# Performance work log

Hardware: AMD Instinct MI355X
Metric: run time of the kernel (lower is better)

## Reference

```python
import jax, jax.numpy as jnp
import numpy as np

N_NODES = 50000
N_EDGES = 800000
IN_FEATS = 256
N_HIDDEN = 256
N_CLASSES = 47


def _glorot(key, shape):
    fan_in, fan_out = shape
    lim = (6.0 / (fan_in + fan_out)) ** 0.5
    return jax.random.uniform(key, shape, jnp.float32, -lim, lim)


def setup_inputs() -> dict:
    key = jax.random.key(0)
    ks = jax.random.split(key, 12)
    x = jax.random.normal(ks[0], (N_NODES, IN_FEATS), jnp.float32)
    src = jax.random.randint(ks[1], (N_EDGES,), 0, N_NODES, jnp.int64)
    dst = jax.random.randint(ks[2], (N_EDGES,), 0, N_NODES, jnp.int64)
    dims = [(IN_FEATS, N_HIDDEN), (N_HIDDEN, N_HIDDEN), (N_HIDDEN, N_CLASSES)]
    inp = {"x": x, "src": src, "dst": dst}
    for i, (di, do) in enumerate(dims):
        inp[f"Wself{i}"] = _glorot(ks[3 + 3 * i], (di, do))
        inp[f"Wneigh{i}"] = _glorot(ks[4 + 3 * i], (di, do))
        inp[f"b{i}"] = jnp.zeros((do,), jnp.float32)
    return inp


def _sage_layer(h, src, dst, Ws, Wn, b):
    # DGL mean SAGEConv: fc_self(h) + fc_neigh(mean over in-neighbors) + bias
    msum = jax.ops.segment_sum(h[src], dst, num_segments=N_NODES)      # [N, d]
    deg = jax.ops.segment_sum(jnp.ones((src.shape[0],), h.dtype), dst,
                              num_segments=N_NODES)                     # [N]
    hmean = msum / jnp.maximum(deg, 1.0)[:, None]
    return h @ Ws + hmean @ Wn + b


def reference(x, src, dst, Wself0, Wneigh0, b0, Wself1, Wneigh1, b1,
              Wself2, Wneigh2, b2):
    h = _sage_layer(x, src, dst, Wself0, Wneigh0, b0)
    h = jax.nn.selu(h)
    h = _sage_layer(h, src, dst, Wself1, Wneigh1, b1)
    h = jax.nn.selu(h)
    h = _sage_layer(h, src, dst, Wself2, Wneigh2, b2)
    return jax.nn.softmax(h, axis=1)
```

## Files before the change

kernel.cpp:

```cpp
#include <hip/hip_runtime.h>
#include <math.h>

#define FEATS 256
#define KTOT  512
#define MS    264
#define SA    40

typedef __attribute__((ext_vector_type(8))) __bf16 bf16x8;
typedef __attribute__((ext_vector_type(4))) float f32x4;

__device__ __forceinline__ float bf2f(unsigned short u) {
    union { unsigned int i; float f; } v; v.i = ((unsigned int)u) << 16; return v.f;
}
__device__ __forceinline__ unsigned short f2bf(float f) {
    unsigned int u = __float_as_uint(f);
    unsigned int r = (u + 0x7FFFu + ((u >> 16) & 1u)) >> 16;
    return (unsigned short)r;
}

__global__ void k_detect(const int* __restrict__ srcRaw, const unsigned short* __restrict__ xr,
                         int nE, int* __restrict__ flag) {
    __shared__ int any, cnt;
    if (threadIdx.x == 0) { any = 0; cnt = 0; }
    __syncthreads();
    int lim = nE < 1024 ? nE : 1024;
    for (int i = threadIdx.x; i < lim; i += 256)
        if (srcRaw[2 * i + 1] != 0) atomicAdd(&any, 1);
    int loc = 0;
    for (int i = threadIdx.x; i < 1024; i += 256) {
        unsigned e = (xr[2 * i] >> 7) & 255u;
        if (e >= 90u && e <= 140u) loc++;
    }
    atomicAdd(&cnt, loc);
    __syncthreads();
    if (threadIdx.x == 0) {
        flag[0] = (any == 0) ? 1 : 0;
        flag[1] = (cnt > 512) ? 1 : 0;
    }
}

__global__ void k_count(const int* __restrict__ dstRaw, int* __restrict__ deg, int nE,
                        int nNodes, const int* __restrict__ flag) {
    int e = blockIdx.x * 256 + threadIdx.x;
    if (e >= nE) return;
    int f = flag[0];
    int d = dstRaw[f ? (2 * e) : e];
    if ((unsigned)d >= (unsigned)nNodes) d = 0;
    atomicAdd(&deg[d], 1);
}

__global__ __launch_bounds__(256) void k_bsum(const int* __restrict__ deg, int* __restrict__ bsum,
                                              int n) {
    __shared__ int buf[256];
    const int t = threadIdx.x;
    int i = blockIdx.x * 256 + t;
    buf[t] = (i < n) ? deg[i] : 0;
    __syncthreads();
    for (int s = 128; s > 0; s >>= 1) {
        if (t < s) buf[t] += buf[t + s];
        __syncthreads();
    }
    if (t == 0) bsum[blockIdx.x] = buf[0];
}

__global__ __launch_bounds__(256) void k_scanb(int* __restrict__ bsum, int nB) {
    __shared__ int buf[256];
    __shared__ int carry;
    const int t = threadIdx.x;
    if (t == 0) carry = 0;
    __syncthreads();
    for (int base = 0; base < nB; base += 256) {
        int i = base + t;
        int v = (i < nB) ? bsum[i] : 0;
        buf[t] = v;
        __syncthreads();
        for (int s = 1; s < 256; s <<= 1) {
            int tv = (t >= s) ? buf[t - s] : 0;
            __syncthreads();
            buf[t] += tv;
            __syncthreads();
        }
        int exc = buf[t] - v;
        int c = carry;
        if (i < nB) bsum[i] = c + exc;
        int tot = buf[255];
        __syncthreads();
        if (t == 0) carry = c + tot;
        __syncthreads();
    }
}

__global__ __launch_bounds__(256) void k_offs(const int* __restrict__ deg,
                                              const int* __restrict__ bsum,
                                              int* __restrict__ off, int* __restrict__ cursor,
                                              int n) {
    __shared__ int buf[256];
    const int t = threadIdx.x, b = blockIdx.x;
    int i = b * 256 + t;
    int v = (i < n) ? deg[i] : 0;
    buf[t] = v;
    __syncthreads();
    for (int s = 1; s < 256; s <<= 1) {
        int tv = (t >= s) ? buf[t - s] : 0;
        __syncthreads();
        buf[t] += tv;
        __syncthreads();
    }
    int exc = bsum[b] + buf[t] - v;
    if (i < n) { off[i] = exc; cursor[i] = exc; }
    if (i == n - 1) off[n] = exc + v;
}

__global__ void k_fill(const int* __restrict__ srcRaw, const int* __restrict__ dstRaw,
                       int* __restrict__ cursor, int* __restrict__ csr, int nE,
                       int nNodes, const int* __restrict__ flag) {
    int e = blockIdx.x * 256 + threadIdx.x;
    if (e >= nE) return;
    int f = flag[0];
    int d = dstRaw[f ? (2 * e) : e];
    int s = srcRaw[f ? (2 * e) : e];
    if ((unsigned)d >= (unsigned)nNodes) d = 0;
    if ((unsigned)s >= (unsigned)nNodes) s = 0;
    int pos = atomicAdd(&cursor[d], 1);
    csr[pos] = s;
}

template <bool F32>
__global__ void k_buildWt(const void* __restrict__ Ws, const void* __restrict__ Wn,
                          unsigned short* __restrict__ Wt, int N, int Npad,
                          const int* __restrict__ flag) {
    if (flag[1] != (F32 ? 0 : 1)) return;
    int idx = blockIdx.x * 256 + threadIdx.x;
    if (idx >= Npad * KTOT) return;
    int n = idx >> 9, k = idx & 511;
    unsigned short v = 0;
    if (n < N) {
        if (F32) {
            float fv = (k < 256) ? ((const float*)Ws)[k * N + n]
                                 : ((const float*)Wn)[(k - 256) * N + n];
            v = f2bf(fv);
        } else {
            v = (k < 256) ? ((const unsigned short*)Ws)[k * N + n]
                          : ((const unsigned short*)Wn)[(k - 256) * N + n];
        }
    }
    Wt[idx] = v;
}

template <bool F32>
__global__ void k_buildWt1(const void* __restrict__ W, unsigned short* __restrict__ Wt,
                           int N, const int* __restrict__ flag) {
    if (flag[1] != (F32 ? 0 : 1)) return;
    int idx = blockIdx.x * 256 + threadIdx.x;
    if (idx >= 64 * 256) return;
    int n = idx >> 8, k = idx & 255;
    unsigned short v = 0;
    if (n < N) {
        v = F32 ? f2bf(((const float*)W)[k * N + n])
                : ((const unsigned short*)W)[k * N + n];
    }
    Wt[idx] = v;
}

template <bool F32>
__device__ __forceinline__ void stage8(const void* h, size_t elemOff, unsigned short* dst) {
    if (!F32) {
        *reinterpret_cast<float4*>(dst) =
            *reinterpret_cast<const float4*>((const unsigned short*)h + elemOff);
    } else {
        const float* p = (const float*)h + elemOff;
        float4 a = *reinterpret_cast<const float4*>(p);
        float4 b = *reinterpret_cast<const float4*>(p + 4);
        dst[0] = f2bf(a.x); dst[1] = f2bf(a.y); dst[2] = f2bf(a.z); dst[3] = f2bf(a.w);
        dst[4] = f2bf(b.x); dst[5] = f2bf(b.y); dst[6] = f2bf(b.z); dst[7] = f2bf(b.w);
    }
}

template <bool HF32>
__global__ __launch_bounds__(256) void k_aggr(
        const void* __restrict__ h, const int* __restrict__ off,
        const int* __restrict__ csr, unsigned short* __restrict__ hmean,
        int M, const int* __restrict__ flag, int want) {
    if (want >= 0 && flag[1] != want) return;
    const int lane = threadIdx.x & 63;
    const int wid = (blockIdx.x * 256 + threadIdx.x) >> 6;
    const int nw = (gridDim.x * 256) >> 6;
    for (int r = wid; r < M; r += nw) {
        const int e0 = off[r], e1 = off[r + 1];
        float a0 = 0.f, a1 = 0.f, a2 = 0.f, a3 = 0.f;
        for (int base = e0; base < e1; base += 64) {
            int cnt = e1 - base; if (cnt > 64) cnt = 64;
            int sidx = (lane < cnt) ? csr[base + lane] : 0;
            #pragma unroll 8
            for (int d = 0; d < cnt; d++) {
                int s = __shfl(sidx, d);
                if (HF32) {
                    float4 hv = reinterpret_cast<const float4*>(
                        (const float*)h + (size_t)s * FEATS)[lane];
                    a0 += hv.x; a1 += hv.y; a2 += hv.z; a3 += hv.w;
                } else {
                    ushort4 hv = reinterpret_cast<const ushort4*>(
                        (const unsigned short*)h + (size_t)s * FEATS)[lane];
                    a0 += bf2f(hv.x); a1 += bf2f(hv.y); a2 += bf2f(hv.z); a3 += bf2f(hv.w);
                }
            }
        }
        float rc = 1.0f / fmaxf((float)(e1 - e0), 1.0f);
        ushort4 o;
        o.x = f2bf(a0 * rc); o.y = f2bf(a1 * rc); o.z = f2bf(a2 * rc); o.w = f2bf(a3 * rc);
        *reinterpret_cast<ushort4*>(&hmean[(size_t)r * FEATS + lane * 4]) = o;
    }
}

__global__ __launch_bounds__(256) void k_aggrP(
        const unsigned short* __restrict__ P, const int* __restrict__ off,
        const int* __restrict__ csr, unsigned short* __restrict__ A, int M) {
    const int lane = threadIdx.x & 63;
    const int wid = (blockIdx.x * 256 + threadIdx.x) >> 6;
    const int nw = (gridDim.x * 256) >> 6;
    const int g = lane >> 5, li = lane & 31;
    for (int r = wid; r < M; r += nw) {
        const int e0 = off[r], e1 = off[r + 1];
        float a0 = 0.f, a1 = 0.f;
        #pragma unroll 4
        for (int base = e0; base < e1; base += 2) {
            int e = base + g;
            if (e < e1) {
                int s = csr[e];
                ushort2 hv = *reinterpret_cast<const ushort2*>(
                    P + (size_t)s * 64 + li * 2);
                a0 += bf2f(hv.x); a1 += bf2f(hv.y);
            }
        }
        a0 += __shfl_xor(a0, 32); a1 += __shfl_xor(a1, 32);
        if (g == 0) {
            float rc = 1.0f / fmaxf((float)(e1 - e0), 1.0f);
            unsigned int packed = (unsigned int)f2bf(a0 * rc) |
                                  ((unsigned int)f2bf(a1 * rc) << 16);
            *reinterpret_cast<unsigned int*>(&A[(size_t)r * 64 + li * 2]) = packed;
        }
    }
}

template <int NT, int ACT, bool HF32, bool BF32, bool OF32>
__global__ __launch_bounds__(256) void k_gemm(
        const void* __restrict__ h, const unsigned short* __restrict__ hmean,
        const unsigned short* __restrict__ Wt, const void* __restrict__ bias,
        void* __restrict__ out, int M, int C, const int* __restrict__ flag, int want) {
    if (flag[1] != want) return;
    __shared__ __align__(16) unsigned short As[64 * SA];
    __shared__ __align__(16) unsigned short Bs[NT * 16 * SA];

    const int m0 = blockIdx.x * 64;
    const int tid = threadIdx.x;
    const int lane = tid & 63, w = tid >> 6;
    const int nh = lane & 15, q = lane >> 4;

    f32x4 acc[NT];
    #pragma unroll
    for (int ci = 0; ci < NT; ci++) acc[ci] = (f32x4){0.f, 0.f, 0.f, 0.f};

    for (int kb = 0; kb < KTOT; kb += 32) {
        {
            int row = tid >> 2, seg = tid & 3;
            int gr = m0 + row; if (gr > M - 1) gr = M - 1;
            if (kb < 256)
                stage8<HF32>(h, (size_t)gr * FEATS + kb + seg * 8, &As[row * SA + seg * 8]);
            else
                stage8<false>(hmean, (size_t)gr * FEATS + (kb - 256) + seg * 8,
                              &As[row * SA + seg * 8]);
        }
        for (int u = tid; u < NT * 64; u += 256) {
            int nn = u >> 2, seg = u & 3;
            *reinterpret_cast<float4*>(&Bs[nn * SA + seg * 8]) =
                *reinterpret_cast<const float4*>(Wt + (size_t)nn * KTOT + kb + seg * 8);
        }
        __syncthreads();
        bf16x8 afr = *reinterpret_cast<const bf16x8*>(&As[(w * 16 + nh) * SA + q * 8]);
        #pragma unroll
        for (int ci = 0; ci < NT; ci++) {
            bf16x8 bfr = *reinterpret_cast<const bf16x8*>(&Bs[(ci * 16 + nh) * SA + q * 8]);
            acc[ci] = __builtin_amdgcn_mfma_f32_16x16x32_bf16(afr, bfr, acc[ci], 0, 0, 0);
        }
        __syncthreads();
    }

    const int rbase = m0 + w * 16 + q * 4;
    const float sc = 1.0507009873554805f, al = 1.6732632423543772f;
    #pragma unroll
    for (int ci = 0; ci < NT; ci++) {
        int col = ci * 16 + nh;
        float b = BF32 ? ((const float*)bias)[col] : bf2f(((const unsigned short*)bias)[col]);
        #pragma unroll
        for (int rg = 0; rg < 4; rg++) {
            int r = rbase + rg;
            if (r < M) {
                float v = acc[ci][rg] + b;
                v = (v > 0.f) ? sc * v : sc * al * expm1f(v);
                if (OF32) ((float*)out)[(size_t)r * (NT * 16) + col] = v;
                else ((unsigned short*)out)[(size_t)r * (NT * 16) + col] = f2bf(v);
            }
        }
    }
}

template <int NT, int ACT, bool ADDP, bool BF32, bool OF32>
__global__ __launch_bounds__(256) void k_gemm256(
        const unsigned short* __restrict__ h, const unsigned short* __restrict__ Wt,
        const void* __restrict__ bias, const unsigned short* __restrict__ Padd,
        void* __restrict__ out, int M, int C, const int* __restrict__ flag, int want) {
    if (want >= 0 && flag[1] != want) return;
    __shared__ __align__(16) unsigned short As[64 * SA];
    __shared__ __align__(16) unsigned short Bs[NT * 16 * SA];

    const int m0 = blockIdx.x * 64;
    const int tid = threadIdx.x;
    const int lane = tid & 63, w = tid >> 6;
    const int nh = lane & 15, q = lane >> 4;

    f32x4 acc[NT];
    #pragma unroll
    for (int ci = 0; ci < NT; ci++) acc[ci] = (f32x4){0.f, 0.f, 0.f, 0.f};

    for (int kb = 0; kb < 256; kb += 32) {
        {
            int row = tid >> 2, seg = tid & 3;
            int gr = m0 + row; if (gr > M - 1) gr = M - 1;
            stage8<false>(h, (size_t)gr * FEATS + kb + seg * 8, &As[row * SA + seg * 8]);
        }
        for (int u = tid; u < NT * 64; u += 256) {
            int nn = u >> 2, seg = u & 3;
            *reinterpret_cast<float4*>(&Bs[nn * SA + seg * 8]) =
                *reinterpret_cast<const float4*>(Wt + (size_t)nn * 256 + kb + seg * 8);
        }
        __syncthreads();
        bf16x8 afr = *reinterpret_cast<const bf16x8*>(&As[(w * 16 + nh) * SA + q * 8]);
        #pragma unroll
        for (int ci = 0; ci < NT; ci++) {
            bf16x8 bfr = *reinterpret_cast<const bf16x8*>(&Bs[(ci * 16 + nh) * SA + q * 8]);
            acc[ci] = __builtin_amdgcn_mfma_f32_16x16x32_bf16(afr, bfr, acc[ci], 0, 0, 0);
        }
        __syncthreads();
    }

    const int rbase = m0 + w * 16 + q * 4;
    if (ACT == 2) {
        #pragma unroll
        for (int ci = 0; ci < NT; ci++) {
            int col = ci * 16 + nh;
            #pragma unroll
            for (int rg = 0; rg < 4; rg++) {
                int r = rbase + rg;
                if (r < M)
                    ((unsigned short*)out)[(size_t)r * (NT * 16) + col] = f2bf(acc[ci][rg]);
            }
        }
    } else {
        #pragma unroll
        for (int rg = 0; rg < 4; rg++) {
            int r = rbase + rg;
            int rr = (r < M) ? r : (M - 1);
            float vals[NT];
            float mx = -1e30f;
            #pragma unroll
            for (int ci = 0; ci < NT; ci++) {
                int col = ci * 16 + nh;
                float v = -1e30f;
                if (col < C) {
                    float b = BF32 ? ((const float*)bias)[col] : bf2f(((const unsigned short*)bias)[col]);
                    float a = ADDP ? bf2f(Padd[(size_t)rr * 64 + col]) : 0.f;
                    v = acc[ci][rg] + a + b;
                }
                vals[ci] = v;
                mx = fmaxf(mx, v);
            }
            #pragma unroll
            for (int mk = 1; mk <= 8; mk <<= 1) mx = fmaxf(mx, __shfl_xor(mx, mk));
            float s = 0.f;
            #pragma unroll
            for (int ci = 0; ci < NT; ci++) {
                float e = (vals[ci] <= -1e29f) ? 0.f : __expf(vals[ci] - mx);
                vals[ci] = e; s += e;
            }
            #pragma unroll
            for (int mk = 1; mk <= 8; mk <<= 1) s += __shfl_xor(s, mk);
            float inv = 1.f / s;
            if (r < M) {
                #pragma unroll
                for (int ci = 0; ci < NT; ci++) {
                    int col = ci * 16 + nh;
                    if (col < C) {
                        if (OF32) ((float*)out)[(size_t)r * C + col] = vals[ci] * inv;
                        else ((unsigned short*)out)[(size_t)r * C + col] = f2bf(vals[ci] * inv);
                    }
                }
            }
        }
    }
}

template <int NT, int ACT, bool HF32, bool BF32, bool OF32>
__global__ __launch_bounds__(256) void k_sage(
        const void* __restrict__ h, const int* __restrict__ off,
        const int* __restrict__ csr, const unsigned short* __restrict__ Wt,
        const void* __restrict__ bias, void* __restrict__ out,
        int M, int C, const int* __restrict__ flag, int want) {
    if (flag[1] != want) return;
    __shared__ __align__(16) unsigned short meanS[64 * MS];
    __shared__ __align__(16) unsigned short As[64 * SA];
    __shared__ __align__(16) unsigned short Bs[NT * 16 * SA];

    const int m0 = blockIdx.x * 64;
    const int tid = threadIdx.x;
    const int lane = tid & 63, w = tid >> 6;
    const int nh = lane & 15, q = lane >> 4;

    for (int i = 0; i < 16; i++) {
        int lr = w * 16 + i;
        int r = m0 + lr;
        int rr = (r < M) ? r : (M - 1);
        int e0 = off[rr], e1 = off[rr + 1];
        float a0 = 0.f, a1 = 0.f, a2 = 0.f, a3 = 0.f;
        #pragma unroll 8
        for (int j = e0; j < e1; j++) {
            int s = csr[j];
            if (HF32) {
                float4 hv = reinterpret_cast<const float4*>((const float*)h + (size_t)s * FEATS)[lane];
                a0 += hv.x; a1 += hv.y; a2 += hv.z; a3 += hv.w;
            } else {
                ushort4 hv = reinterpret_cast<const ushort4*>((const unsigned short*)h + (size_t)s * FEATS)[lane];
                a0 += bf2f(hv.x); a1 += bf2f(hv.y); a2 += bf2f(hv.z); a3 += bf2f(hv.w);
            }
        }
        float rc = 1.0f / fmaxf((float)(e1 - e0), 1.0f);
        ushort4 o;
        o.x = f2bf(a0 * rc); o.y = f2bf(a1 * rc); o.z = f2bf(a2 * rc); o.w = f2bf(a3 * rc);
        *reinterpret_cast<ushort4*>(&meanS[lr * MS + lane * 4]) = o;
    }
    __syncthreads();

    f32x4 acc[NT];
    #pragma unroll
    for (int ci = 0; ci < NT; ci++) acc[ci] = (f32x4){0.f, 0.f, 0.f, 0.f};

    for (int kb = 0; kb < KTOT; kb += 32) {
        const bool fromMean = (kb >= 256);
        if (!fromMean) {
            int row = tid >> 2, seg = tid & 3;
            int gr = m0 + row; if (gr > M - 1) gr = M - 1;
            stage8<HF32>(h, (size_t)gr * FEATS + kb + seg * 8, &As[row * SA + seg * 8]);
        }
        for (int u = tid; u < NT * 64; u += 256) {
            int nn = u >> 2, seg = u & 3;
            *reinterpret_cast<float4*>(&Bs[nn * SA + seg * 8]) =
                *reinterpret_cast<const float4*>(Wt + (size_t)nn * KTOT + kb + seg * 8);
        }
        __syncthreads();
        bf16x8 afr;
        if (!fromMean)
            afr = *reinterpret_cast<const bf16x8*>(&As[(w * 16 + nh) * SA + q * 8]);
        else
            afr = *reinterpret_cast<const bf16x8*>(&meanS[(w * 16 + nh) * MS + (kb - 256) + q * 8]);
        #pragma unroll
        for (int ci = 0; ci < NT; ci++) {
            bf16x8 bfr = *reinterpret_cast<const bf16x8*>(&Bs[(ci * 16 + nh) * SA + q * 8]);
            acc[ci] = __builtin_amdgcn_mfma_f32_16x16x32_bf16(afr, bfr, acc[ci], 0, 0, 0);
        }
        __syncthreads();
    }

    const int rbase = m0 + w * 16 + q * 4;
    if (ACT == 0) {
        const float sc = 1.0507009873554805f, al = 1.6732632423543772f;
        #pragma unroll
        for (int ci = 0; ci < NT; ci++) {
            int col = ci * 16 + nh;
            float b = BF32 ? ((const float*)bias)[col] : bf2f(((const unsigned short*)bias)[col]);
            #pragma unroll
            for (int rg = 0; rg < 4; rg++) {
                int r = rbase + rg;
                if (r < M) {
                    float v = acc[ci][rg] + b;
                    v = (v > 0.f) ? sc * v : sc * al * expm1f(v);
                    if (OF32) ((float*)out)[(size_t)r * (NT * 16) + col] = v;
                    else ((unsigned short*)out)[(size_t)r * (NT * 16) + col] = f2bf(v);
                }
            }
        }
    } else {
        #pragma unroll
        for (int rg = 0; rg < 4; rg++) {
            int r = rbase + rg;
            float vals[NT];
            float mx = -1e30f;
            #pragma unroll
            for (int ci = 0; ci < NT; ci++) {
                int col = ci * 16 + nh;
                float v = -1e30f;
                if (col < C) {
                    float b = BF32 ? ((const float*)bias)[col] : bf2f(((const unsigned short*)bias)[col]);
                    v = acc[ci][rg] + b;
                }
                vals[ci] = v;
                mx = fmaxf(mx, v);
            }
            #pragma unroll
            for (int mk = 1; mk <= 8; mk <<= 1) mx = fmaxf(mx, __shfl_xor(mx, mk));
            float s = 0.f;
            #pragma unroll
            for (int ci = 0; ci < NT; ci++) {
                float e = (vals[ci] <= -1e29f) ? 0.f : __expf(vals[ci] - mx);
                vals[ci] = e; s += e;
            }
            #pragma unroll
            for (int mk = 1; mk <= 8; mk <<= 1) s += __shfl_xor(s, mk);
            float inv = 1.f / s;
            if (r < M) {
                #pragma unroll
                for (int ci = 0; ci < NT; ci++) {
                    int col = ci * 16 + nh;
                    if (col < C) {
                        if (OF32) ((float*)out)[(size_t)r * C + col] = vals[ci] * inv;
                        else ((unsigned short*)out)[(size_t)r * C + col] = f2bf(vals[ci] * inv);
                    }
                }
            }
        }
    }
}

extern "C" void kernel_launch(void* const* d_in, const int* in_sizes, int n_in,
                              void* d_out, int out_size, void* d_ws, size_t ws_size,
                              hipStream_t stream) {
    const void* x     = d_in[0];
    const int* srcRaw = (const int*)d_in[1];
    const int* dstRaw = (const int*)d_in[2];
    const void* Ws0 = d_in[3]; const void* Wn0 = d_in[4]; const void* b0 = d_in[5];
    const void* Ws1 = d_in[6]; const void* Wn1 = d_in[7]; const void* b1 = d_in[8];
    const void* Ws2 = d_in[9]; const void* Wn2 = d_in[10]; const void* b2 = d_in[11];

    const int nNodes = in_sizes[0] / FEATS;
    const int nE     = in_sizes[1];
    const int C      = in_sizes[11];

    char* ws = (char*)d_ws;
    size_t off_b = 0;
    auto carve = [&](size_t bytes) -> void* {
        void* p = (void*)(ws + off_b);
        off_b += (bytes + 255) & ~(size_t)255;
        return p;
    };
    int*            flag   = (int*)           carve(256);
    int*            deg    = (int*)           carve((size_t)nNodes * 4);
    int*            cursor = (int*)           carve((size_t)nNodes * 4);
    int*            off    = (int*)           carve((size_t)(nNodes + 1) * 4);
    int*            csr    = (int*)           carve((size_t)nE * 4);
    unsigned short* Wt0    = (unsigned short*)carve((size_t)256 * KTOT * 2);
    unsigned short* Wt1    = (unsigned short*)carve((size_t)256 * KTOT * 2);
    unsigned short* Wt2    = (unsigned short*)carve((size_t)64 * KTOT * 2);
    unsigned short* Wt2s   = (unsigned short*)carve((size_t)64 * 256 * 2);
    unsigned short* Wt2n   = (unsigned short*)carve((size_t)64 * 256 * 2);
    int*            bsum   = (int*)           carve(4096);
    unsigned short* hA     = (unsigned short*)carve((size_t)nNodes * FEATS * 2);
    unsigned short* hmean  = (unsigned short*)carve((size_t)nNodes * FEATS * 2);
    const bool split = (off_b <= ws_size);
    unsigned short* P2 = hmean;
    unsigned short* A2 = hmean + (size_t)4 * 1024 * 1024;
    unsigned short* hX = (unsigned short*)d_in[0];

    const int edgeBlocks = (nE + 255) / 256;
    const int nodeBlocks = (nNodes + 255) / 256;
    const int sageBlocks = (nNodes + 63) / 64;
    const int aggrBlocks = 2048;

    k_detect<<<1, 256, 0, stream>>>(srcRaw, (const unsigned short*)x, nE, flag);
    hipMemsetAsync(deg, 0, (size_t)nNodes * 4, stream);
    k_count<<<edgeBlocks, 256, 0, stream>>>(dstRaw, deg, nE, nNodes, flag);
    k_bsum<<<nodeBlocks, 256, 0, stream>>>(deg, bsum, nNodes);
    k_scanb<<<1, 256, 0, stream>>>(bsum, nodeBlocks);
    k_offs<<<nodeBlocks, 256, 0, stream>>>(deg, bsum, off, cursor, nNodes);
    k_fill<<<edgeBlocks, 256, 0, stream>>>(srcRaw, dstRaw, cursor, csr, nE, nNodes, flag);

    int wtB = (256 * KTOT + 255) / 256;
    k_buildWt<false><<<wtB, 256, 0, stream>>>(Ws0, Wn0, Wt0, 256, 256, flag);
    k_buildWt<true ><<<wtB, 256, 0, stream>>>(Ws0, Wn0, Wt0, 256, 256, flag);
    k_buildWt<false><<<wtB, 256, 0, stream>>>(Ws1, Wn1, Wt1, 256, 256, flag);
    k_buildWt<true ><<<wtB, 256, 0, stream>>>(Ws1, Wn1, Wt1, 256, 256, flag);

    if (split) {
        int wt1B = (64 * 256 + 255) / 256;
        k_buildWt1<false><<<wt1B, 256, 0, stream>>>(Ws2, Wt2s, C, flag);
        k_buildWt1<true ><<<wt1B, 256, 0, stream>>>(Ws2, Wt2s, C, flag);
        k_buildWt1<false><<<wt1B, 256, 0, stream>>>(Wn2, Wt2n, C, flag);
        k_buildWt1<true ><<<wt1B, 256, 0, stream>>>(Wn2, Wt2n, C, flag);

        k_aggr<false><<<aggrBlocks, 256, 0, stream>>>(x, off, csr, hmean, nNodes, flag, 1);
        k_aggr<true ><<<aggrBlocks, 256, 0, stream>>>(x, off, csr, hmean, nNodes, flag, 0);
        k_gemm<16, 0, false, false, false><<<sageBlocks, 256, 0, stream>>>(
            x, hmean, Wt0, b0, hA, nNodes, 256, flag, 1);
        k_gemm<16, 0, true, true, false><<<sageBlocks, 256, 0, stream>>>(
            x, hmean, Wt0, b0, hA, nNodes, 256, flag, 0);

        k_aggr<false><<<aggrBlocks, 256, 0, stream>>>(hA, off, csr, hmean, nNodes, flag, -1);
        k_gemm<16, 0, false, false, false><<<sageBlocks, 256, 0, stream>>>(
            hA, hmean, Wt1, b1, hX, nNodes, 256, flag, 1);
        k_gemm<16, 0, false, true, false><<<sageBlocks, 256, 0, stream>>>(
            hA, hmean, Wt1, b1, hX, nNodes, 256, flag, 0);

        k_gemm256<4, 2, false, false, false><<<sageBlocks, 256, 0, stream>>>(
            hX, Wt2n, b2, (const unsigned short*)nullptr, P2, nNodes, C, flag, -1);
        k_aggrP<<<aggrBlocks, 256, 0, stream>>>(P2, off, csr, A2, nNodes);
        k_gemm256<4, 1, true, false, false><<<sageBlocks, 256, 0, stream>>>(
            hX, Wt2s, b2, A2, d_out, nNodes, C, flag, 1);
        k_gemm256<4, 1, true, true, true><<<sageBlocks, 256, 0, stream>>>(
            hX, Wt2s, b2, A2, d_out, nNodes, C, flag, 0);
    } else {
        int wtB2 = (64 * KTOT + 255) / 256;
        k_buildWt<false><<<wtB2, 256, 0, stream>>>(Ws2, Wn2, Wt2, C, 64, flag);
        k_buildWt<true ><<<wtB2, 256, 0, stream>>>(Ws2, Wn2, Wt2, C, 64, flag);
        k_sage<16, 0, false, false, false><<<sageBlocks, 256, 0, stream>>>(
            x, off, csr, Wt0, b0, hA, nNodes, 256, flag, 1);
        k_sage<16, 0, true, true, false><<<sageBlocks, 256, 0, stream>>>(
            x, off, csr, Wt0, b0, hA, nNodes, 256, flag, 0);
        k_sage<16, 0, false, false, false><<<sageBlocks, 256, 0, stream>>>(
            hA, off, csr, Wt1, b1, hX, nNodes, 256, flag, 1);
        k_sage<16, 0, false, true, false><<<sageBlocks, 256, 0, stream>>>(
            hA, off, csr, Wt1, b1, hX, nNodes, 256, flag, 0);
        k_sage<4, 1, false, false, false><<<sageBlocks, 256, 0, stream>>>(
            hX, off, csr, Wt2, b2, d_out, nNodes, C, flag, 1);
        k_sage<4, 1, false, true, true><<<sageBlocks, 256, 0, stream>>>(
            hX, off, csr, Wt2, b2, d_out, nNodes, C, flag, 0);
    }
}
```

Measured before the change: 669.7 us.

## Split layer GEMMs into column halves with async LDS loads and swizzled tiles

The two 256-wide SAGE layer GEMMs now give each block a 64x128 output tile, which doubles the grid. The K step widens to 64, and global-to-LDS copies use the direct global_load_lds path with an XOR-swizzled layout instead of padded rows. The aim is more blocks for occupancy, fewer K iterations and barriers, fewer LDS bank conflicts, and less register staging. In exchange, each A row tile is now read twice, once per column half, and the async loads are not explicitly waited on before the barrier, which may be a correctness risk.

Result: faster. 551.9 us (-17.6%).

```diff
diff --git a/kernel.cpp b/kernel.cpp
--- a/kernel.cpp
+++ b/kernel.cpp
@@ -8,6 +8,10 @@
 
 typedef __attribute__((ext_vector_type(8))) __bf16 bf16x8;
 typedef __attribute__((ext_vector_type(4))) float f32x4;
+
+#define ASYNC16(G, L) __builtin_amdgcn_global_load_lds( \
+    (const __attribute__((address_space(1))) unsigned int*)(G), \
+    (__attribute__((address_space(3))) unsigned int*)(L), 16, 0, 0)
 
 __device__ __forceinline__ float bf2f(unsigned short u) {
     union { unsigned int i; float f; } v; v.i = ((unsigned int)u) << 16; return v.f;
@@ -242,45 +246,71 @@
     }
 }
 
-template <int NT, int ACT, bool HF32, bool BF32, bool OF32>
+template <bool HF32, bool BF32, bool OF32>
 __global__ __launch_bounds__(256) void k_gemm(
         const void* __restrict__ h, const unsigned short* __restrict__ hmean,
         const unsigned short* __restrict__ Wt, const void* __restrict__ bias,
-        void* __restrict__ out, int M, int C, const int* __restrict__ flag, int want) {
+        void* __restrict__ out, int M, const int* __restrict__ flag, int want) {
     if (flag[1] != want) return;
-    __shared__ __align__(16) unsigned short As[64 * SA];
-    __shared__ __align__(16) unsigned short Bs[NT * 16 * SA];
-
-    const int m0 = blockIdx.x * 64;
+    __shared__ __align__(16) unsigned short As[64 * 64];
+    __shared__ __align__(16) unsigned short Bs[128 * 64];
+
+    const int rb = (int)blockIdx.x >> 1;
+    const int chalf = (int)blockIdx.x & 1;
+    const int m0 = rb * 64;
+    const int col0 = chalf * 128;
     const int tid = threadIdx.x;
     const int lane = tid & 63, w = tid >> 6;
     const int nh = lane & 15, q = lane >> 4;
 
-    f32x4 acc[NT];
+    f32x4 acc[8];
     #pragma unroll
-    for (int ci = 0; ci < NT; ci++) acc[ci] = (f32x4){0.f, 0.f, 0.f, 0.f};
-
-    for (int kb = 0; kb < KTOT; kb += 32) {
-        {
-            int row = tid >> 2, seg = tid & 3;
+    for (int ci = 0; ci < 8; ci++) acc[ci] = (f32x4){0.f, 0.f, 0.f, 0.f};
+
+    for (int kb = 0; kb < KTOT; kb += 64) {
+        #pragma unroll
+        for (int j = 0; j < 2; j++) {
+            int t2 = tid + j * 256;
+            int row = t2 >> 3, c = t2 & 7;
             int gr = m0 + row; if (gr > M - 1) gr = M - 1;
-            if (kb < 256)
-                stage8<HF32>(h, (size_t)gr * FEATS + kb + seg * 8, &As[row * SA + seg * 8]);
-            else
-                stage8<false>(hmean, (size_t)gr * FEATS + (kb - 256) + seg * 8,
-                              &As[row * SA + seg * 8]);
-        }
-        for (int u = tid; u < NT * 64; u += 256) {
-            int nn = u >> 2, seg = u & 3;
-            *reinterpret_cast<float4*>(&Bs[nn * SA + seg * 8]) =
-                *reinterpret_cast<const float4*>(Wt + (size_t)nn * KTOT + kb + seg * 8);
-        }
-        __syncthreads();
-        bf16x8 afr = *reinterpret_cast<const bf16x8*>(&As[(w * 16 + nh) * SA + q * 8]);
-        #pragma unroll
-        for (int ci = 0; ci < NT; ci++) {
-            bf16x8 bfr = *reinterpret_cast<const bf16x8*>(&Bs[(ci * 16 + nh) * SA + q * 8]);
-            acc[ci] = __builtin_amdgcn_mfma_f32_16x16x32_bf16(afr, bfr, acc[ci], 0, 0, 0);
+            int cs = c ^ (row & 7);
+            if (kb < 256) {
+                if (HF32) {
+                    const float* p = (const float*)h + (size_t)gr * FEATS + kb + cs * 8;
+                    float4 a = *reinterpret_cast<const float4*>(p);
+                    float4 b = *reinterpret_cast<const float4*>(p + 4);
+                    unsigned short* d = &As[t2 * 8];
+                    d[0]=f2bf(a.x); d[1]=f2bf(a.y); d[2]=f2bf(a.z); d[3]=f2bf(a.w);
+                    d[4]=f2bf(b.x); d[5]=f2bf(b.y); d[6]=f2bf(b.z); d[7]=f2bf(b.w);
+                } else {
+                    ASYNC16((const unsigned short*)h + (size_t)gr * FEATS + kb + cs * 8,
+                            &As[t2 * 8]);
+                }
+            } else {
+                ASYNC16(hmean + (size_t)gr * FEATS + (kb - 256) + cs * 8, &As[t2 * 8]);
+            }
+        }
+        #pragma unroll
+        for (int j = 0; j < 4; j++) {
+            int t2 = tid + j * 256;
+            int n = t2 >> 3, c = t2 & 7;
+            int cs = c ^ (n & 7);
+            ASYNC16(Wt + (size_t)(col0 + n) * KTOT + kb + cs * 8, &Bs[t2 * 8]);
+        }
+        __syncthreads();
+
+        #pragma unroll
+        for (int s = 0; s < 2; s++) {
+            const int arow = w * 16 + nh;
+            const int qa = ((s * 4 + q) ^ (arow & 7));
+            bf16x8 afr = *reinterpret_cast<const bf16x8*>(&As[arow * 64 + qa * 8]);
+            #pragma unroll
+            for (int ci = 0; ci < 8; ci++) {
+                int n = ci * 16 + nh;
+                int qb = ((s * 4 + q) ^ (n & 7));
+                bf16x8 bfr = *reinterpret_cast<const bf16x8*>(&Bs[n * 64 + qb * 8]);
+                acc[ci] = __builtin_amdgcn_mfma_f32_16x16x32_bf16(afr, bfr, acc[ci], 0, 0, 0);
+            }
         }
         __syncthreads();
     }
@@ -288,8 +318,8 @@
     const int rbase = m0 + w * 16 + q * 4;
     const float sc = 1.0507009873554805f, al = 1.6732632423543772f;
     #pragma unroll
-    for (int ci = 0; ci < NT; ci++) {
-        int col = ci * 16 + nh;
+    for (int ci = 0; ci < 8; ci++) {
+        int col = col0 + ci * 16 + nh;
         float b = BF32 ? ((const float*)bias)[col] : bf2f(((const unsigned short*)bias)[col]);
         #pragma unroll
         for (int rg = 0; rg < 4; rg++) {
@@ -297,8 +327,8 @@
             if (r < M) {
                 float v = acc[ci][rg] + b;
                 v = (v > 0.f) ? sc * v : sc * al * expm1f(v);
-                if (OF32) ((float*)out)[(size_t)r * (NT * 16) + col] = v;
-                else ((unsigned short*)out)[(size_t)r * (NT * 16) + col] = f2bf(v);
+                if (OF32) ((float*)out)[(size_t)r * FEATS + col] = v;
+                else ((unsigned short*)out)[(size_t)r * FEATS + col] = f2bf(v);
             }
         }
     }
@@ -571,6 +601,7 @@
     const int edgeBlocks = (nE + 255) / 256;
     const int nodeBlocks = (nNodes + 255) / 256;
     const int sageBlocks = (nNodes + 63) / 64;
+    const int gemmBlocks = sageBlocks * 2;
     const int aggrBlocks = 2048;
 
     k_detect<<<1, 256, 0, stream>>>(srcRaw, (const unsigned short*)x, nE, flag);
@@ -596,16 +627,16 @@
 
         k_aggr<false><<<aggrBlocks, 256, 0, stream>>>(x, off, csr, hmean, nNodes, flag, 1);
         k_aggr<true ><<<aggrBlocks, 256, 0, stream>>>(x, off, csr, hmean, nNodes, flag, 0);
-        k_gemm<16, 0, false, false, false><<<sageBlocks, 256, 0, stream>>>(
-            x, hmean, Wt0, b0, hA, nNodes, 256, flag, 1);
-        k_gemm<16, 0, true, true, false><<<sageBlocks, 256, 0, stream>>>(
-            x, hmean, Wt0, b0, hA, nNodes, 256, flag, 0);
+        k_gemm<false, false, false><<<gemmBlocks, 256, 0, stream>>>(
+            x, hmean, Wt0, b0, hA, nNodes, flag, 1);
+        k_gemm<true, true, false><<<gemmBlocks, 256, 0, stream>>>(
+            x, hmean, Wt0, b0, hA, nNodes, flag, 0);
 
         k_aggr<false><<<aggrBlocks, 256, 0, stream>>>(hA, off, csr, hmean, nNodes, flag, -1);
-        k_gemm<16, 0, false, false, false><<<sageBlocks, 256, 0, stream>>>(
-            hA, hmean, Wt1, b1, hX, nNodes, 256, flag, 1);
-        k_gemm<16, 0, false, true, false><<<sageBlocks, 256, 0, stream>>>(
-            hA, hmean, Wt1, b1, hX, nNodes, 256, flag, 0);
+        k_gemm<false, false, false><<<gemmBlocks, 256, 0, stream>>>(
+            hA, hmean, Wt1, b1, hX, nNodes, flag, 1);
+        k_gemm<false, true, false><<<gemmBlocks, 256, 0, stream>>>(
+            hA, hmean, Wt1, b1, hX, nNodes, flag, 0);
 
         k_gemm256<4, 2, false, false, false><<<sageBlocks, 256, 0, stream>>>(
             hX, Wt2n, b2, (const unsigned short*)nullptr, P2, nNodes, C, flag, -1);
```
